# Kernel optimization log

Hardware: AMD Instinct MI355X
Metric: run time of the kernel (lower is better)

The kernel has to match this reference:

```python
import jax, jax.numpy as jnp
import numpy as np

D_OUT = 10
N_BINS = 50
DELTA_SCALE = 60.0
TEMPERATURE = 1.0
CAND_BATCH = 1000  # hard-coded in the torch forward loop
EPS = 1e-8


def setup_inputs() -> dict:
    key = jax.random.key(0)
    ks = jax.random.split(key, 7)
    n_q, n_c, d_num, d_cat = 512, 8000, 6, 20
    return {
        "x_num": jax.random.normal(ks[0], (n_q, d_num), dtype=jnp.float32),
        "x_cat": jax.random.uniform(ks[1], (n_q, d_cat), dtype=jnp.float32),
        "candidate_x_num": jax.random.normal(ks[2], (n_c, d_num), dtype=jnp.float32),
        "candidate_x_cat": jax.random.uniform(ks[3], (n_c, d_cat), dtype=jnp.float32),
        "candidate_y": jax.random.randint(ks[4], (n_c,), 0, D_OUT, dtype=jnp.int64),
        # delta = rand(d_in_num, n_bins) * delta_scale (Parameter init)
        "delta": jax.random.uniform(ks[5], (d_num, N_BINS), dtype=jnp.float32) * DELTA_SCALE,
        # u = rand(d_in_num, n_bins) (buffer)
        "u": jax.random.uniform(ks[6], (d_num, N_BINS), dtype=jnp.float32),
    }


def _feature_map(x, delta, u):
    # x: [N, d_num] -> bin indices [N, d_num * n_bins]
    scaled_u = u * delta  # [d_num, n_bins]
    bins = jnp.ceil((x[:, :, None] - scaled_u[None]) / delta[None])
    return bins.reshape(x.shape[0], -1)


def reference(x_num, x_cat, candidate_x_num, candidate_x_cat, candidate_y, delta, u):
    x_enc = jnp.concatenate([_feature_map(x_num, delta, u), x_cat], axis=1)          # [Nq, D]
    c_enc = jnp.concatenate([_feature_map(candidate_x_num, delta, u), candidate_x_cat], axis=1)  # [Nc, D]
    y_oh = jax.nn.one_hot(candidate_y, D_OUT, dtype=jnp.float32)                     # [Nc, d_out]

    n_c, d = c_enc.shape
    n_chunks = n_c // CAND_BATCH
    c_chunks = c_enc.reshape(n_chunks, CAND_BATCH, d)
    y_chunks = y_oh.reshape(n_chunks, CAND_BATCH, D_OUT)

    def step(carry, batch):
        logits, lse = carry
        cx, cy = batch
        # L1 cdist: [Nq, CAND_BATCH]
        dist = jnp.sum(jnp.abs(x_enc[:, None, :] - cx[None, :, :]), axis=-1) / TEMPERATURE
        logits = logits + jnp.exp(-dist) @ cy
        # NOTE: faithful to torch code — per-batch logsumexp values are SUMMED
        lse = lse + jax.nn.logsumexp(-dist, axis=1)
        return (logits, lse), None

    n_q = x_enc.shape[0]
    init = (jnp.zeros((n_q, D_OUT), jnp.float32), jnp.zeros((n_q,), jnp.float32))
    (logits, lse), _ = jax.lax.scan(step, init, (c_chunks, y_chunks))
    return jnp.log(logits + EPS) - lse[:, None]
```

## Files before the change

kernel.cpp:

```cpp
#include <hip/hip_runtime.h>
#include <math.h>

#define NQ 512
#define NC 8000
#define DNUM 6
#define NBINS 50
#define DCAT 20
#define DENC 26
#define DOUT 10
#define CHUNK 1000
#define NCHUNK 8
#define SPLIT 4
#define SUBC 250
#define QT 4

__global__ void encode(const float* __restrict__ c_num, const float* __restrict__ c_cat,
                       const float* __restrict__ x_num, const float* __restrict__ x_cat,
                       const float* __restrict__ delta, const float* __restrict__ u,
                       float* __restrict__ cEnc, float* __restrict__ qEnc,
                       float* __restrict__ g_logits) {
    int i = blockIdx.x * 256 + threadIdx.x;
    const int nA = (NC + NQ) * DNUM;
    const int nB = (NC + NQ) * DCAT;
    if (i < nA) {
        int f = i % DNUM, p = i / DNUM;
        bool is_c = p < NC;
        int idx = is_c ? p : p - NC;
        float v = (is_c ? c_num : x_num)[idx * DNUM + f];
        float g = 0.f;
        for (int j = 0; j < NBINS; ++j) {
            float dl = delta[f * NBINS + j];
            float sc = u[f * NBINS + j] * dl;
            g += ceilf((v - sc) / dl);
        }
        if (is_c) cEnc[f * NC + idx] = g;
        else      qEnc[f * NQ + idx] = g;
    } else if (i < nA + nB) {
        int i2 = i - nA;
        int k = i2 % DCAT, p = i2 / DCAT;
        bool is_c = p < NC;
        int idx = is_c ? p : p - NC;
        float v = (is_c ? c_cat : x_cat)[idx * DCAT + k];
        if (is_c) cEnc[(DNUM + k) * NC + idx] = v;
        else      qEnc[(DNUM + k) * NQ + idx] = v;
    } else {
        int i3 = i - nA - nB;
        if (i3 < NQ * DOUT) g_logits[i3] = 0.f;
    }
}

__global__ __launch_bounds__(256) void nca_main(
    const float* __restrict__ cEnc, const float* __restrict__ qEnc,
    const int* __restrict__ cy,
    float* __restrict__ g_logits, float* __restrict__ parts) {
    __shared__ float qs[DENC * QT];
    __shared__ float lds_logits[QT * DOUT];
    __shared__ float wred[QT * 4];
    __shared__ float m_sh[QT];

    const int tid = threadIdx.x;
    const int chunk = blockIdx.x / SPLIT;
    const int sub = blockIdx.x % SPLIT;
    const int q0 = blockIdx.y * QT;

    if (tid < DENC * QT) {
        int d = tid >> 2, q = tid & 3;
        qs[tid] = qEnc[d * NQ + q0 + q];
    }
    if (tid < QT * DOUT) lds_logits[tid] = 0.f;
    __syncthreads();

    const bool active = (tid < SUBC);
    const int cl = chunk * CHUNK + sub * SUBC + (active ? tid : SUBC - 1);
    const float* cp = cEnc + cl;

    float acc[QT] = {0.f, 0.f, 0.f, 0.f};
#pragma unroll
    for (int d = 0; d < DENC; ++d) {
        float cv = cp[(size_t)d * NC];
        float4 xq = *(const float4*)(qs + d * QT);
        acc[0] += fabsf(cv - xq.x);
        acc[1] += fabsf(cv - xq.y);
        acc[2] += fabsf(cv - xq.z);
        acc[3] += fabsf(cv - xq.w);
    }

    if (active) {
        int y = cy[cl];
#pragma unroll
        for (int q = 0; q < QT; ++q)
            atomicAdd(&lds_logits[q * DOUT + y], __expf(-acc[q]));
    }

    const int lane = tid & 63, wave = tid >> 6;

#pragma unroll
    for (int q = 0; q < QT; ++q) {
        float v = active ? acc[q] : INFINITY;
#pragma unroll
        for (int m = 32; m >= 1; m >>= 1) v = fminf(v, __shfl_xor(v, m));
        if (lane == 0) wred[q * 4 + wave] = v;
    }
    __syncthreads();
    if (tid < QT) {
        float m = wred[tid * 4];
#pragma unroll
        for (int w = 1; w < 4; ++w) m = fminf(m, wred[tid * 4 + w]);
        m_sh[tid] = m;
    }
    __syncthreads();

#pragma unroll
    for (int q = 0; q < QT; ++q) {
        float s = active ? __expf(m_sh[q] - acc[q]) : 0.f;
#pragma unroll
        for (int mm = 32; mm >= 1; mm >>= 1) s += __shfl_xor(s, mm);
        if (lane == 0) wred[q * 4 + wave] = s;
    }
    __syncthreads();
    if (tid < QT) {
        float s = 0.f;
#pragma unroll
        for (int w = 0; w < 4; ++w) s += wred[tid * 4 + w];
        int qg = q0 + tid;
        float2 ms = make_float2(m_sh[tid], s);
        *(float2*)(parts + 2 * (((size_t)qg * NCHUNK + chunk) * SPLIT + sub)) = ms;
    }
    __syncthreads();
    if (tid < QT * DOUT)
        atomicAdd(&g_logits[q0 * DOUT + tid], lds_logits[tid]);
}

__global__ void finalize(const float* __restrict__ g_logits, const float* __restrict__ parts,
                         float* __restrict__ out) {
    int q = blockIdx.x * 256 + threadIdx.x;
    if (q >= NQ) return;
    float lse = 0.f;
    for (int ch = 0; ch < NCHUNK; ++ch) {
        const float* p = parts + 2 * (((size_t)q * NCHUNK + ch) * SPLIT);
        float M = INFINITY;
#pragma unroll
        for (int s = 0; s < SPLIT; ++s) M = fminf(M, p[2 * s]);
        float S = 0.f;
#pragma unroll
        for (int s = 0; s < SPLIT; ++s) S += __expf(M - p[2 * s]) * p[2 * s + 1];
        lse += logf(S) - M;
    }
#pragma unroll
    for (int k = 0; k < DOUT; ++k)
        out[q * DOUT + k] = logf(g_logits[q * DOUT + k] + 1e-8f) - lse;
}

extern "C" void kernel_launch(void* const* d_in, const int* in_sizes, int n_in,
                              void* d_out, int out_size, void* d_ws, size_t ws_size,
                              hipStream_t stream) {
    const float* x_num = (const float*)d_in[0];
    const float* x_cat = (const float*)d_in[1];
    const float* c_num = (const float*)d_in[2];
    const float* c_cat = (const float*)d_in[3];
    const int*   c_y   = (const int*)d_in[4];
    const float* delta = (const float*)d_in[5];
    const float* u     = (const float*)d_in[6];

    float* ws = (float*)d_ws;
    float* cEnc = ws;
    float* qEnc = cEnc + (size_t)DENC * NC;
    float* g_logits = qEnc + (size_t)DENC * NQ;
    float* parts = g_logits + NQ * DOUT;

    const int total = (NC + NQ) * (DNUM + DCAT) + NQ * DOUT;
    encode<<<(total + 255) / 256, 256, 0, stream>>>(
        c_num, c_cat, x_num, x_cat, delta, u, cEnc, qEnc, g_logits);
    nca_main<<<dim3(NCHUNK * SPLIT, NQ / QT), 256, 0, stream>>>(
        cEnc, qEnc, c_y, g_logits, parts);
    finalize<<<(NQ + 255) / 256, 256, 0, stream>>>(g_logits, parts, (float*)d_out);
}
```

Baseline: 112.1 us.

## Double queries per block and keep candidate features in registers

Query encodings are now stored row-major with a padded stride of 32. The main kernel reads them straight from global memory with block-uniform addresses instead of staging them in LDS. Each thread holds all 26 candidate features in registers and scores 8 queries instead of 4, which halves the number of blocks and the redundant candidate loads and per-block setup. The cost is more registers per thread, a stated occupancy target of 8 blocks per SM, and twice the per-query reduction work inside each block.

New measurement: 111.9 us. Within noise of the previous version (-0.2%).

```diff
diff --git a/kernel.cpp b/kernel.cpp
--- a/kernel.cpp
+++ b/kernel.cpp
@@ -7,12 +7,13 @@
 #define NBINS 50
 #define DCAT 20
 #define DENC 26
+#define QSTRIDE 32
 #define DOUT 10
 #define CHUNK 1000
 #define NCHUNK 8
 #define SPLIT 4
 #define SUBC 250
-#define QT 4
+#define QT 8
 
 __global__ void encode(const float* __restrict__ c_num, const float* __restrict__ c_cat,
                        const float* __restrict__ x_num, const float* __restrict__ x_cat,
@@ -34,7 +35,7 @@
             g += ceilf((v - sc) / dl);
         }
         if (is_c) cEnc[f * NC + idx] = g;
-        else      qEnc[f * NQ + idx] = g;
+        else      qEnc[idx * QSTRIDE + f] = g;
     } else if (i < nA + nB) {
         int i2 = i - nA;
         int k = i2 % DCAT, p = i2 / DCAT;
@@ -42,18 +43,17 @@
         int idx = is_c ? p : p - NC;
         float v = (is_c ? c_cat : x_cat)[idx * DCAT + k];
         if (is_c) cEnc[(DNUM + k) * NC + idx] = v;
-        else      qEnc[(DNUM + k) * NQ + idx] = v;
+        else      qEnc[idx * QSTRIDE + DNUM + k] = v;
     } else {
         int i3 = i - nA - nB;
         if (i3 < NQ * DOUT) g_logits[i3] = 0.f;
     }
 }
 
-__global__ __launch_bounds__(256) void nca_main(
+__global__ __launch_bounds__(256, 8) void nca_main(
     const float* __restrict__ cEnc, const float* __restrict__ qEnc,
     const int* __restrict__ cy,
     float* __restrict__ g_logits, float* __restrict__ parts) {
-    __shared__ float qs[DENC * QT];
     __shared__ float lds_logits[QT * DOUT];
     __shared__ float wred[QT * 4];
     __shared__ float m_sh[QT];
@@ -63,26 +63,24 @@
     const int sub = blockIdx.x % SPLIT;
     const int q0 = blockIdx.y * QT;
 
-    if (tid < DENC * QT) {
-        int d = tid >> 2, q = tid & 3;
-        qs[tid] = qEnc[d * NQ + q0 + q];
-    }
     if (tid < QT * DOUT) lds_logits[tid] = 0.f;
     __syncthreads();
 
     const bool active = (tid < SUBC);
     const int cl = chunk * CHUNK + sub * SUBC + (active ? tid : SUBC - 1);
-    const float* cp = cEnc + cl;
 
-    float acc[QT] = {0.f, 0.f, 0.f, 0.f};
+    float cv[DENC];
 #pragma unroll
-    for (int d = 0; d < DENC; ++d) {
-        float cv = cp[(size_t)d * NC];
-        float4 xq = *(const float4*)(qs + d * QT);
-        acc[0] += fabsf(cv - xq.x);
-        acc[1] += fabsf(cv - xq.y);
-        acc[2] += fabsf(cv - xq.z);
-        acc[3] += fabsf(cv - xq.w);
+    for (int d = 0; d < DENC; ++d) cv[d] = cEnc[(size_t)d * NC + cl];
+
+    float acc[QT];
+#pragma unroll
+    for (int q = 0; q < QT; ++q) {
+        const float* qp = qEnc + (size_t)(q0 + q) * QSTRIDE;
+        float a = 0.f;
+#pragma unroll
+        for (int d = 0; d < DENC; ++d) a += fabsf(cv[d] - qp[d]);
+        acc[q] = a;
     }
 
     if (active) {
@@ -165,7 +163,7 @@
     float* ws = (float*)d_ws;
     float* cEnc = ws;
     float* qEnc = cEnc + (size_t)DENC * NC;
-    float* g_logits = qEnc + (size_t)DENC * NQ;
+    float* g_logits = qEnc + (size_t)NQ * QSTRIDE;
     float* parts = g_logits + NQ * DOUT;
 
     const int total = (NC + NQ) * (DNUM + DCAT) + NQ * DOUT;
```
